# Optimization experiments

Measured on AMD Instinct MI355X. Metric: run time of the kernel, lower is better.

The kernel has to match this reference:

```python
import jax, jax.numpy as jnp
import numpy as np

HIDDEN = 256
NUM_STEPS = 3
N_NODES = 200000
N_GRAPHS = 512


def setup_inputs() -> dict:
    key = jax.random.key(0)
    ks = jax.random.split(key, 8)
    h = HIDDEN
    x = jax.random.normal(ks[0], (N_NODES, h), dtype=jnp.float32)
    batch = jnp.sort(jax.random.randint(ks[1], (N_NODES,), 0, N_GRAPHS)).astype(jnp.int64)
    s_ih = 1.0 / np.sqrt(2 * h)
    s_hh = 1.0 / np.sqrt(h)
    # LSTM (input 2h -> hidden h), PyTorch gate order i,f,g,o
    W_ih = jax.random.uniform(ks[2], (4 * h, 2 * h), jnp.float32, -s_ih, s_ih)
    W_hh = jax.random.uniform(ks[3], (4 * h, h), jnp.float32, -s_hh, s_hh)
    b_ih = jax.random.uniform(ks[4], (4 * h,), jnp.float32, -s_hh, s_hh)
    b_hh = jax.random.uniform(ks[5], (4 * h,), jnp.float32, -s_hh, s_hh)
    # out_proj: Linear(2h -> h)
    s_o = 1.0 / np.sqrt(2 * h)
    W_out = jax.random.uniform(ks[6], (h, 2 * h), jnp.float32, -s_o, s_o)
    b_out = jax.random.uniform(ks[7], (h,), jnp.float32, -s_o, s_o)
    return {"x": x, "batch": batch, "W_ih": W_ih, "W_hh": W_hh,
            "b_ih": b_ih, "b_hh": b_hh, "W_out": W_out, "b_out": b_out,
            "n_graphs": N_GRAPHS}


def _set2set(x, batch, W_ih, W_hh, b_ih, b_hh, n_graphs):
    h = x.shape[1]
    hs = jnp.zeros((n_graphs, h), x.dtype)
    cs = jnp.zeros((n_graphs, h), x.dtype)
    q_star = jnp.zeros((n_graphs, 2 * h), x.dtype)
    for _ in range(NUM_STEPS):
        # LSTM step (PyTorch gate order: i, f, g, o)
        gates = q_star @ W_ih.T + hs @ W_hh.T + (b_ih + b_hh)  # [B, 4h]
        i_g, f_g, g_g, o_g = jnp.split(gates, 4, axis=-1)
        cs = jax.nn.sigmoid(f_g) * cs + jax.nn.sigmoid(i_g) * jnp.tanh(g_g)
        hs = jax.nn.sigmoid(o_g) * jnp.tanh(cs)
        q = hs  # [B, h]
        # attention logits per node
        e = jnp.sum(x * q[batch], axis=-1)  # [N]
        # segment softmax over nodes of each graph
        m = jax.ops.segment_max(e, batch, num_segments=n_graphs)
        a = jnp.exp(e - m[batch])
        denom = jax.ops.segment_sum(a, batch, num_segments=n_graphs)
        a = a / denom[batch]
        # weighted readout
        r = jax.ops.segment_sum(a[:, None] * x, batch, num_segments=n_graphs)  # [B, h]
        q_star = jnp.concatenate([q, r], axis=-1)  # [B, 2h]
    return q_star


def reference(x, batch, W_ih, W_hh, b_ih, b_hh, W_out, b_out, n_graphs):
    q_star = _set2set(x, batch.astype(jnp.int32), W_ih, W_hh, b_ih, b_hh, n_graphs)
    return q_star @ W_out.T + b_out
```

## Files before the change

kernel.cpp:

```cpp
#include <hip/hip_runtime.h>
#include <hip/hip_bf16.h>

#define HID 256
#define NG 512

__device__ __forceinline__ float sigmoidf_(float v) { return 1.f / (1.f + __expf(-v)); }

__global__ __launch_bounds__(256) void prep_kernel(
    const float* __restrict__ W_ih, const float* __restrict__ W_hh,
    const float* __restrict__ b_ih, const float* __restrict__ b_hh,
    float* __restrict__ Wcat, float* __restrict__ bcat)
{
    int idx = blockIdx.x * 256 + threadIdx.x;
    if (idx < 1024 * 512) {
        int k = idx & 511;
        float v = W_ih[idx];
        if (k < 256) v += W_hh[(idx >> 9) * 256 + k];
        Wcat[idx] = v;
    }
    if (idx < 1024) bcat[idx] = b_ih[idx] + b_hh[idx];
}

__global__ __launch_bounds__(256) void find_starts(
    const int* __restrict__ batch, int n, int* __restrict__ starts)
{
    int g = blockIdx.x * 256 + threadIdx.x;
    if (g > NG) return;
    if (g == NG) { starts[NG] = n; return; }
    int lo = 0, hi = n;
    while (lo < hi) {
        int mid = (lo + hi) >> 1;
        if (batch[mid] < g) lo = mid + 1; else hi = mid;
    }
    starts[g] = lo;
}

__global__ __launch_bounds__(256) void attn_kernel(
    const float* __restrict__ x, const int* __restrict__ starts,
    const float* __restrict__ gp0, const float* __restrict__ gp1,
    const float* __restrict__ bcat, float* __restrict__ cs,
    float* __restrict__ qs, int step0)
{
    __shared__ __align__(16) float ql[HID];
    __shared__ __align__(16) float red[4][HID];
    __shared__ float mw[4], lw[4];

    const int g = blockIdx.x;
    const int tid = threadIdx.x;

    float ig, fg, gg, og, cp;
    if (step0) {
        ig = bcat[tid]; fg = bcat[256 + tid]; gg = bcat[512 + tid]; og = bcat[768 + tid];
        cp = 0.f;
    } else {
        const float* a0 = gp0 + (size_t)g * 1024;
        const float* a1 = gp1 + (size_t)g * 1024;
        ig = a0[tid]       + a1[tid]       + bcat[tid];
        fg = a0[256 + tid] + a1[256 + tid] + bcat[256 + tid];
        gg = a0[512 + tid] + a1[512 + tid] + bcat[512 + tid];
        og = a0[768 + tid] + a1[768 + tid] + bcat[768 + tid];
        cp = cs[g * HID + tid];
    }
    float cn = sigmoidf_(fg) * cp + sigmoidf_(ig) * tanhf(gg);
    float h  = sigmoidf_(og) * tanhf(cn);
    cs[g * HID + tid] = cn;
    qs[(size_t)g * 512 + tid] = h;
    ql[tid] = h;

    const int s0 = starts[g];
    const int nn = starts[g + 1] - s0;
    if (nn <= 0) { qs[(size_t)g * 512 + HID + tid] = 0.f; return; }
    __syncthreads();

    const int w = tid >> 6, lane = tid & 63;
    const int j = lane >> 3;
    const int s = lane & 7;

    float4 qf[8];
    #pragma unroll
    for (int k = 0; k < 8; ++k) qf[k] = *(const float4*)&ql[k * 32 + s * 4];

    const int nch = (nn + 7) >> 3;
    const int last = s0 + nn - 1;
    const float NEG = -3.402823466e38f;

    float m_run = NEG, l_run = 0.f;
    float4 racc[8] = {};
    float4 xc[8], xn[8];

    int c = w;
    if (c < nch) {
        int node = s0 + c * 8 + j; if (node > last) node = last;
        const float* bp = x + (size_t)node * HID + s * 4;
        #pragma unroll
        for (int k = 0; k < 8; ++k) xc[k] = *(const float4*)(bp + k * 32);
    }
    for (; c < nch; c += 4) {
        if (c + 4 < nch) {
            int node = s0 + (c + 4) * 8 + j; if (node > last) node = last;
            const float* bp = x + (size_t)node * HID + s * 4;
            #pragma unroll
            for (int k = 0; k < 8; ++k) xn[k] = *(const float4*)(bp + k * 32);
        }
        const bool valid = (c * 8 + j) < nn;

        float e = 0.f;
        #pragma unroll
        for (int k = 0; k < 8; ++k)
            e += xc[k].x * qf[k].x + xc[k].y * qf[k].y + xc[k].z * qf[k].z + xc[k].w * qf[k].w;
        e += __shfl_xor(e, 1); e += __shfl_xor(e, 2); e += __shfl_xor(e, 4);
        e = valid ? e : NEG;

        float mc = e;
        mc = fmaxf(mc, __shfl_xor(mc, 8));
        mc = fmaxf(mc, __shfl_xor(mc, 16));
        mc = fmaxf(mc, __shfl_xor(mc, 32));
        float m_new = fmaxf(m_run, mc);
        float alpha = __expf(m_run - m_new);
        float p = valid ? __expf(e - m_new) : 0.f;
        float ps = p;
        ps += __shfl_xor(ps, 8); ps += __shfl_xor(ps, 16); ps += __shfl_xor(ps, 32);
        l_run = l_run * alpha + ps;
        m_run = m_new;
        #pragma unroll
        for (int k = 0; k < 8; ++k) {
            racc[k].x = racc[k].x * alpha + p * xc[k].x;
            racc[k].y = racc[k].y * alpha + p * xc[k].y;
            racc[k].z = racc[k].z * alpha + p * xc[k].z;
            racc[k].w = racc[k].w * alpha + p * xc[k].w;
        }
        #pragma unroll
        for (int k = 0; k < 8; ++k) xc[k] = xn[k];
    }

    #pragma unroll
    for (int k = 0; k < 8; ++k) {
        racc[k].x += __shfl_xor(racc[k].x, 8);
        racc[k].y += __shfl_xor(racc[k].y, 8);
        racc[k].z += __shfl_xor(racc[k].z, 8);
        racc[k].w += __shfl_xor(racc[k].w, 8);
        racc[k].x += __shfl_xor(racc[k].x, 16);
        racc[k].y += __shfl_xor(racc[k].y, 16);
        racc[k].z += __shfl_xor(racc[k].z, 16);
        racc[k].w += __shfl_xor(racc[k].w, 16);
        racc[k].x += __shfl_xor(racc[k].x, 32);
        racc[k].y += __shfl_xor(racc[k].y, 32);
        racc[k].z += __shfl_xor(racc[k].z, 32);
        racc[k].w += __shfl_xor(racc[k].w, 32);
    }
    if (j == 0) {
        #pragma unroll
        for (int k = 0; k < 8; ++k) *(float4*)&red[w][k * 32 + s * 4] = racc[k];
        if (s == 0) { mw[w] = m_run; lw[w] = l_run; }
    }
    __syncthreads();

    float M = fmaxf(fmaxf(mw[0], mw[1]), fmaxf(mw[2], mw[3]));
    float f0 = __expf(mw[0] - M), f1 = __expf(mw[1] - M);
    float f2 = __expf(mw[2] - M), f3 = __expf(mw[3] - M);
    float L = lw[0] * f0 + lw[1] * f1 + lw[2] * f2 + lw[3] * f3;
    float r = red[0][tid] * f0 + red[1][tid] * f1 + red[2][tid] * f2 + red[3][tid] * f3;
    qs[(size_t)g * 512 + HID + tid] = r / L;
}

__global__ __launch_bounds__(256) void gemm_splitk(
    const float* __restrict__ A, int lda,
    const float* __restrict__ B, int ldb,
    float* __restrict__ Cp, int ldc, int KS, size_t slice_stride)
{
    __shared__ float As[16][76];
    __shared__ float Bs[16][76];
    const int tid = threadIdx.x;
    const int tx = tid & 15, ty = tid >> 4;
    const int m0 = blockIdx.y * 64, n0 = blockIdx.x * 64;
    const int kb = blockIdx.z * KS;
    const int r = tid >> 2, kc = (tid & 3) << 2;
    float acc[4][4] = {};

    const float* Ap = &A[(size_t)(m0 + r) * lda + kb + kc];
    const float* Bp = &B[(size_t)(n0 + r) * ldb + kb + kc];
    float4 av = *(const float4*)Ap;
    float4 bv = *(const float4*)Bp;

    for (int k0 = 0; k0 < KS; k0 += 16) {
        As[kc + 0][r] = av.x; As[kc + 1][r] = av.y; As[kc + 2][r] = av.z; As[kc + 3][r] = av.w;
        Bs[kc + 0][r] = bv.x; Bs[kc + 1][r] = bv.y; Bs[kc + 2][r] = bv.z; Bs[kc + 3][r] = bv.w;
        __syncthreads();
        if (k0 + 16 < KS) {
            av = *(const float4*)(Ap + k0 + 16);
            bv = *(const float4*)(Bp + k0 + 16);
        }
        #pragma unroll
        for (int kk = 0; kk < 16; ++kk) {
            float4 a = *(const float4*)&As[kk][ty << 2];
            float4 b = *(const float4*)&Bs[kk][tx << 2];
            acc[0][0] += a.x * b.x; acc[0][1] += a.x * b.y; acc[0][2] += a.x * b.z; acc[0][3] += a.x * b.w;
            acc[1][0] += a.y * b.x; acc[1][1] += a.y * b.y; acc[1][2] += a.y * b.z; acc[1][3] += a.y * b.w;
            acc[2][0] += a.z * b.x; acc[2][1] += a.z * b.y; acc[2][2] += a.z * b.z; acc[2][3] += a.z * b.w;
            acc[3][0] += a.w * b.x; acc[3][1] += a.w * b.y; acc[3][2] += a.w * b.z; acc[3][3] += a.w * b.w;
        }
        __syncthreads();
    }
    float* out = Cp + blockIdx.z * slice_stride;
    #pragma unroll
    for (int i = 0; i < 4; ++i) {
        float4 o = make_float4(acc[i][0], acc[i][1], acc[i][2], acc[i][3]);
        *(float4*)&out[(size_t)(m0 + ty * 4 + i) * ldc + n0 + (tx << 2)] = o;
    }
}

__global__ __launch_bounds__(256) void finalize_out(
    const float* __restrict__ op, const float* __restrict__ b_out,
    float* __restrict__ out)
{
    int i = blockIdx.x * 256 + threadIdx.x;
    if (i < 512 * 256) {
        float v = op[i] + op[131072 + i] + op[262144 + i] + op[393216 + i] + b_out[i & 255];
        out[i] = v;
    }
}

extern "C" void kernel_launch(void* const* d_in, const int* in_sizes, int n_in,
                              void* d_out, int out_size, void* d_ws, size_t ws_size,
                              hipStream_t stream)
{
    const float* x     = (const float*)d_in[0];
    const int*   batch = (const int*)d_in[1];
    const float* W_ih  = (const float*)d_in[2];
    const float* W_hh  = (const float*)d_in[3];
    const float* b_ih  = (const float*)d_in[4];
    const float* b_hh  = (const float*)d_in[5];
    const float* W_out = (const float*)d_in[6];
    const float* b_out = (const float*)d_in[7];
    float* out = (float*)d_out;
    const int n = in_sizes[1];
    (void)n_in; (void)out_size; (void)ws_size;

    char* ws = (char*)d_ws;
    float* qs      = (float*)(ws);
    float* cs      = (float*)(ws + 0x100000);
    float* gates_p = (float*)(ws + 0x180000);
    float* Wcat    = (float*)(ws + 0x580000);
    float* bcat    = (float*)(ws + 0x780000);
    int*   starts  = (int*)  (ws + 0x781000);
    float* out_p   = (float*)(ws + 0x790000);

    prep_kernel<<<2048, 256, 0, stream>>>(W_ih, W_hh, b_ih, b_hh, Wcat, bcat);
    find_starts<<<3, 256, 0, stream>>>(batch, n, starts);

    for (int step = 0; step < 3; ++step) {
        if (step > 0) {
            gemm_splitk<<<dim3(16, 8, 2), 256, 0, stream>>>(
                qs, 512, Wcat, 512, gates_p, 1024, 256, (size_t)512 * 1024);
        }
        attn_kernel<<<NG, 256, 0, stream>>>(
            x, starts, gates_p, gates_p + (size_t)512 * 1024, bcat, cs, qs, step == 0);
    }
    gemm_splitk<<<dim3(4, 8, 4), 256, 0, stream>>>(
        qs, 512, W_out, 512, out_p, 256, 128, (size_t)512 * 256);
    finalize_out<<<512, 256, 0, stream>>>(out_p, b_out, out);
}
```

Measured before the change: 415.3 us.

## Double attention block to 512 threads, split gate GEMM 4-way, merge setup kernels

The attention kernel now runs 8 wavefronts per graph instead of 4. Each wave streams every eighth chunk of nodes, and an 8-way online-softmax merge combines the partial results. To free registers, the query vector is read from shared memory inside the dot product instead of being kept in registers. The gate GEMM split-K goes from 2 to 4 slices to expose more blocks, the workspace is reshuffled to fit four partial slices, and the two setup kernels are merged into one launch. The extra waves should hide more memory latency per graph, at the cost of more LDS reads, a larger reduction and more partial-sum traffic.

```diff
diff --git a/kernel.cpp b/kernel.cpp
--- a/kernel.cpp
+++ b/kernel.cpp
@@ -1,84 +1,86 @@
 #include <hip/hip_runtime.h>
-#include <hip/hip_bf16.h>
 
 #define HID 256
 #define NG 512
 
 __device__ __forceinline__ float sigmoidf_(float v) { return 1.f / (1.f + __expf(-v)); }
 
-__global__ __launch_bounds__(256) void prep_kernel(
+__global__ __launch_bounds__(256) void setup_kernel(
     const float* __restrict__ W_ih, const float* __restrict__ W_hh,
     const float* __restrict__ b_ih, const float* __restrict__ b_hh,
-    float* __restrict__ Wcat, float* __restrict__ bcat)
-{
-    int idx = blockIdx.x * 256 + threadIdx.x;
-    if (idx < 1024 * 512) {
+    float* __restrict__ Wcat, float* __restrict__ bcat,
+    const int* __restrict__ batch, int n, int* __restrict__ starts)
+{
+    int b = blockIdx.x;
+    if (b < 2048) {
+        int idx = b * 256 + threadIdx.x;
         int k = idx & 511;
         float v = W_ih[idx];
         if (k < 256) v += W_hh[(idx >> 9) * 256 + k];
         Wcat[idx] = v;
-    }
-    if (idx < 1024) bcat[idx] = b_ih[idx] + b_hh[idx];
-}
-
-__global__ __launch_bounds__(256) void find_starts(
-    const int* __restrict__ batch, int n, int* __restrict__ starts)
-{
-    int g = blockIdx.x * 256 + threadIdx.x;
-    if (g > NG) return;
-    if (g == NG) { starts[NG] = n; return; }
-    int lo = 0, hi = n;
-    while (lo < hi) {
-        int mid = (lo + hi) >> 1;
-        if (batch[mid] < g) lo = mid + 1; else hi = mid;
-    }
-    starts[g] = lo;
-}
-
-__global__ __launch_bounds__(256) void attn_kernel(
+        if (idx < 1024) bcat[idx] = b_ih[idx] + b_hh[idx];
+    } else {
+        int g = (b - 2048) * 256 + threadIdx.x;
+        if (g > NG) return;
+        if (g == NG) { starts[NG] = n; return; }
+        int lo = 0, hi = n;
+        while (lo < hi) {
+            int mid = (lo + hi) >> 1;
+            if (batch[mid] < g) lo = mid + 1; else hi = mid;
+        }
+        starts[g] = lo;
+    }
+}
+
+__global__ __launch_bounds__(512, 4) void attn_kernel(
     const float* __restrict__ x, const int* __restrict__ starts,
-    const float* __restrict__ gp0, const float* __restrict__ gp1,
+    const float* __restrict__ gates_p,
     const float* __restrict__ bcat, float* __restrict__ cs,
     float* __restrict__ qs, int step0)
 {
     __shared__ __align__(16) float ql[HID];
-    __shared__ __align__(16) float red[4][HID];
-    __shared__ float mw[4], lw[4];
+    __shared__ __align__(16) float red[8][HID];
+    __shared__ float mw[8], lw[8];
 
     const int g = blockIdx.x;
     const int tid = threadIdx.x;
 
-    float ig, fg, gg, og, cp;
-    if (step0) {
-        ig = bcat[tid]; fg = bcat[256 + tid]; gg = bcat[512 + tid]; og = bcat[768 + tid];
-        cp = 0.f;
-    } else {
-        const float* a0 = gp0 + (size_t)g * 1024;
-        const float* a1 = gp1 + (size_t)g * 1024;
-        ig = a0[tid]       + a1[tid]       + bcat[tid];
-        fg = a0[256 + tid] + a1[256 + tid] + bcat[256 + tid];
-        gg = a0[512 + tid] + a1[512 + tid] + bcat[512 + tid];
-        og = a0[768 + tid] + a1[768 + tid] + bcat[768 + tid];
-        cp = cs[g * HID + tid];
-    }
-    float cn = sigmoidf_(fg) * cp + sigmoidf_(ig) * tanhf(gg);
-    float h  = sigmoidf_(og) * tanhf(cn);
-    cs[g * HID + tid] = cn;
-    qs[(size_t)g * 512 + tid] = h;
-    ql[tid] = h;
+    if (tid < 256) {
+        float ig, fg, gg, og, cp;
+        if (step0) {
+            ig = bcat[tid]; fg = bcat[256 + tid]; gg = bcat[512 + tid]; og = bcat[768 + tid];
+            cp = 0.f;
+        } else {
+            ig = bcat[tid]; fg = bcat[256 + tid]; gg = bcat[512 + tid]; og = bcat[768 + tid];
+            const float* a = gates_p + (size_t)g * 1024;
+            const size_t ss = (size_t)512 * 1024;
+            #pragma unroll
+            for (int z = 0; z < 4; ++z) {
+                const float* az = a + z * ss;
+                ig += az[tid]; fg += az[256 + tid]; gg += az[512 + tid]; og += az[768 + tid];
+            }
+            cp = cs[g * HID + tid];
+        }
+        float cn = sigmoidf_(fg) * cp + sigmoidf_(ig) * tanhf(gg);
+        float h  = sigmoidf_(og) * tanhf(cn);
+        cs[g * HID + tid] = cn;
+        qs[(size_t)g * 512 + tid] = h;
+        ql[tid] = h;
+    }
+    __syncthreads();
 
     const int s0 = starts[g];
     const int nn = starts[g + 1] - s0;
-    if (nn <= 0) { qs[(size_t)g * 512 + HID + tid] = 0.f; return; }
-    __syncthreads();
+    if (nn <= 0) {
+        if (tid < 256) qs[(size_t)g * 512 + HID + tid] = 0.f;
+        return;
+    }
 
     const int w = tid >> 6, lane = tid & 63;
     const int j = lane >> 3;
     const int s = lane & 7;
 
-    float4 qf[8];
-    #pragma unroll
-    for (int k = 0; k < 8; ++k) qf[k] = *(const float4*)&ql[k * 32 + s * 4];
+    const float4* qp = (const float4*)&ql[s * 4];
 
     const int nch = (nn + 7) >> 3;
     const int last = s0 + nn - 1;
@@ -95,9 +97,9 @@
         #pragma unroll
         for (int k = 0; k < 8; ++k) xc[k] = *(const float4*)(bp + k * 32);
     }
-    for (; c < nch; c += 4) {
-        if (c + 4 < nch) {
-            int node = s0 + (c + 4) * 8 + j; if (node > last) node = last;
+    for (; c < nch; c += 8) {
+        if (c + 8 < nch) {
+            int node = s0 + (c + 8) * 8 + j; if (node > last) node = last;
             const float* bp = x + (size_t)node * HID + s * 4;
             #pragma unroll
             for (int k = 0; k < 8; ++k) xn[k] = *(const float4*)(bp + k * 32);
@@ -106,8 +108,10 @@
 
         float e = 0.f;
         #pragma unroll
-        for (int k = 0; k < 8; ++k)
-            e += xc[k].x * qf[k].x + xc[k].y * qf[k].y + xc[k].z * qf[k].z + xc[k].w * qf[k].w;
+        for (int k = 0; k < 8; ++k) {
+            float4 q = qp[k * 8];
+            e += xc[k].x * q.x + xc[k].y * q.y + xc[k].z * q.z + xc[k].w * q.w;
+        }
         e += __shfl_xor(e, 1); e += __shfl_xor(e, 2); e += __shfl_xor(e, 4);
         e = valid ? e : NEG;
 
@@ -155,12 +159,19 @@
     }
     __syncthreads();
 
-    float M = fmaxf(fmaxf(mw[0], mw[1]), fmaxf(mw[2], mw[3]));
-    float f0 = __expf(mw[0] - M), f1 = __expf(mw[1] - M);
-    float f2 = __expf(mw[2] - M), f3 = __expf(mw[3] - M);
-    float L = lw[0] * f0 + lw[1] * f1 + lw[2] * f2 + lw[3] * f3;
-    float r = red[0][tid] * f0 + red[1][tid] * f1 + red[2][tid] * f2 + red[3][tid] * f3;
-    qs[(size_t)g * 512 + HID + tid] = r / L;
+    if (tid < 256) {
+        float M = NEG;
+        #pragma unroll
+        for (int v = 0; v < 8; ++v) M = fmaxf(M, mw[v]);
+        float L = 0.f, r = 0.f;
+        #pragma unroll
+        for (int v = 0; v < 8; ++v) {
+            float f = __expf(mw[v] - M);
+            L += lw[v] * f;
+            r += red[v][tid] * f;
+        }
+        qs[(size_t)g * 512 + HID + tid] = r / L;
+    }
 }
 
 __global__ __launch_bounds__(256) void gemm_splitk(
@@ -240,21 +251,21 @@
     float* qs      = (float*)(ws);
     float* cs      = (float*)(ws + 0x100000);
     float* gates_p = (float*)(ws + 0x180000);
-    float* Wcat    = (float*)(ws + 0x580000);
-    float* bcat    = (float*)(ws + 0x780000);
-    int*   starts  = (int*)  (ws + 0x781000);
-    float* out_p   = (float*)(ws + 0x790000);
-
-    prep_kernel<<<2048, 256, 0, stream>>>(W_ih, W_hh, b_ih, b_hh, Wcat, bcat);
-    find_starts<<<3, 256, 0, stream>>>(batch, n, starts);
+    float* Wcat    = (float*)(ws + 0x980000);
+    float* bcat    = (float*)(ws + 0xB80000);
+    int*   starts  = (int*)  (ws + 0xB81000);
+    float* out_p   = (float*)(ws + 0xB90000);
+
+    setup_kernel<<<2051, 256, 0, stream>>>(W_ih, W_hh, b_ih, b_hh, Wcat, bcat,
+                                           batch, n, starts);
 
     for (int step = 0; step < 3; ++step) {
         if (step > 0) {
-            gemm_splitk<<<dim3(16, 8, 2), 256, 0, stream>>>(
-                qs, 512, Wcat, 512, gates_p, 1024, 256, (size_t)512 * 1024);
-        }
-        attn_kernel<<<NG, 256, 0, stream>>>(
-            x, starts, gates_p, gates_p + (size_t)512 * 1024, bcat, cs, qs, step == 0);
+            gemm_splitk<<<dim3(16, 8, 4), 256, 0, stream>>>(
+                qs, 512, Wcat, 512, gates_p, 1024, 128, (size_t)512 * 1024);
+        }
+        attn_kernel<<<NG, 512, 0, stream>>>(
+            x, starts, gates_p, bcat, cs, qs, step == 0);
     }
     gemm_splitk<<<dim3(4, 8, 4), 256, 0, stream>>>(
         qs, 512, W_out, 512, out_p, 256, 128, (size_t)512 * 256);
```

Result: slower. 491.2 us (+18.3%).

## Split fused online-softmax attention into separate logit, softmax and readout kernels

Applied to the files above, without the earlier changes.

Replaces the single-pass online-softmax attention kernel with three kernels. The first computes per-node logits, the second does the segment max and sum and writes normalized weights, and the third accumulates the weighted readout. This removes the per-chunk rescaling and shuffle reductions from the inner loop. In exchange x is read twice per step, two extra launches are added per step, and e/a buffers make a round trip through memory. Prep and find_starts are also merged into one setup kernel to drop a launch.

```diff
diff --git a/kernel.cpp b/kernel.cpp
--- a/kernel.cpp
+++ b/kernel.cpp
@@ -1,75 +1,70 @@
 #include <hip/hip_runtime.h>
-#include <hip/hip_bf16.h>
 
 #define HID 256
 #define NG 512
 
 __device__ __forceinline__ float sigmoidf_(float v) { return 1.f / (1.f + __expf(-v)); }
 
-__global__ __launch_bounds__(256) void prep_kernel(
+__global__ __launch_bounds__(256) void setup_kernel(
     const float* __restrict__ W_ih, const float* __restrict__ W_hh,
     const float* __restrict__ b_ih, const float* __restrict__ b_hh,
-    float* __restrict__ Wcat, float* __restrict__ bcat)
-{
-    int idx = blockIdx.x * 256 + threadIdx.x;
-    if (idx < 1024 * 512) {
+    float* __restrict__ Wcat, float* __restrict__ bcat,
+    const int* __restrict__ batch, int n, int* __restrict__ starts)
+{
+    int b = blockIdx.x;
+    if (b < 2048) {
+        int idx = b * 256 + threadIdx.x;
         int k = idx & 511;
         float v = W_ih[idx];
         if (k < 256) v += W_hh[(idx >> 9) * 256 + k];
         Wcat[idx] = v;
-    }
-    if (idx < 1024) bcat[idx] = b_ih[idx] + b_hh[idx];
-}
-
-__global__ __launch_bounds__(256) void find_starts(
-    const int* __restrict__ batch, int n, int* __restrict__ starts)
-{
-    int g = blockIdx.x * 256 + threadIdx.x;
-    if (g > NG) return;
-    if (g == NG) { starts[NG] = n; return; }
-    int lo = 0, hi = n;
-    while (lo < hi) {
-        int mid = (lo + hi) >> 1;
-        if (batch[mid] < g) lo = mid + 1; else hi = mid;
-    }
-    starts[g] = lo;
-}
-
-__global__ __launch_bounds__(256) void attn_kernel(
+        if (idx < 1024) bcat[idx] = b_ih[idx] + b_hh[idx];
+    } else {
+        int g = (b - 2048) * 256 + threadIdx.x;
+        if (g > NG) return;
+        if (g == NG) { starts[NG] = n; return; }
+        int lo = 0, hi = n;
+        while (lo < hi) {
+            int mid = (lo + hi) >> 1;
+            if (batch[mid] < g) lo = mid + 1; else hi = mid;
+        }
+        starts[g] = lo;
+    }
+}
+
+__global__ __launch_bounds__(256) void e_kernel(
     const float* __restrict__ x, const int* __restrict__ starts,
-    const float* __restrict__ gp0, const float* __restrict__ gp1,
+    const float* __restrict__ gates_p,
     const float* __restrict__ bcat, float* __restrict__ cs,
-    float* __restrict__ qs, int step0)
+    float* __restrict__ qs, float* __restrict__ e, int step0)
 {
     __shared__ __align__(16) float ql[HID];
-    __shared__ __align__(16) float red[4][HID];
-    __shared__ float mw[4], lw[4];
 
     const int g = blockIdx.x;
     const int tid = threadIdx.x;
 
-    float ig, fg, gg, og, cp;
-    if (step0) {
-        ig = bcat[tid]; fg = bcat[256 + tid]; gg = bcat[512 + tid]; og = bcat[768 + tid];
-        cp = 0.f;
-    } else {
-        const float* a0 = gp0 + (size_t)g * 1024;
-        const float* a1 = gp1 + (size_t)g * 1024;
-        ig = a0[tid]       + a1[tid]       + bcat[tid];
-        fg = a0[256 + tid] + a1[256 + tid] + bcat[256 + tid];
-        gg = a0[512 + tid] + a1[512 + tid] + bcat[512 + tid];
-        og = a0[768 + tid] + a1[768 + tid] + bcat[768 + tid];
-        cp = cs[g * HID + tid];
-    }
-    float cn = sigmoidf_(fg) * cp + sigmoidf_(ig) * tanhf(gg);
-    float h  = sigmoidf_(og) * tanhf(cn);
-    cs[g * HID + tid] = cn;
-    qs[(size_t)g * 512 + tid] = h;
-    ql[tid] = h;
+    {
+        float ig = bcat[tid], fg = bcat[256 + tid], gg = bcat[512 + tid], og = bcat[768 + tid];
+        float cp = 0.f;
+        if (!step0) {
+            const float* a0 = gates_p + (size_t)g * 1024;
+            const float* a1 = a0 + (size_t)512 * 1024;
+            ig += a0[tid]       + a1[tid];
+            fg += a0[256 + tid] + a1[256 + tid];
+            gg += a0[512 + tid] + a1[512 + tid];
+            og += a0[768 + tid] + a1[768 + tid];
+            cp = cs[g * HID + tid];
+        }
+        float cn = sigmoidf_(fg) * cp + sigmoidf_(ig) * tanhf(gg);
+        float h  = sigmoidf_(og) * tanhf(cn);
+        cs[g * HID + tid] = cn;
+        qs[(size_t)g * 512 + tid] = h;
+        ql[tid] = h;
+    }
 
     const int s0 = starts[g];
     const int nn = starts[g + 1] - s0;
-    if (nn <= 0) { qs[(size_t)g * 512 + HID + tid] = 0.f; return; }
+    if (nn <= 0) return;
     __syncthreads();
 
     const int w = tid >> 6, lane = tid & 63;
@@ -82,12 +77,8 @@
 
     const int nch = (nn + 7) >> 3;
     const int last = s0 + nn - 1;
-    const float NEG = -3.402823466e38f;
-
-    float m_run = NEG, l_run = 0.f;
-    float4 racc[8] = {};
+
     float4 xc[8], xn[8];
-
     int c = w;
     if (c < nch) {
         int node = s0 + c * 8 + j; if (node > last) node = last;
@@ -102,35 +93,96 @@
             #pragma unroll
             for (int k = 0; k < 8; ++k) xn[k] = *(const float4*)(bp + k * 32);
         }
-        const bool valid = (c * 8 + j) < nn;
-
-        float e = 0.f;
+        float ev = 0.f;
         #pragma unroll
         for (int k = 0; k < 8; ++k)
-            e += xc[k].x * qf[k].x + xc[k].y * qf[k].y + xc[k].z * qf[k].z + xc[k].w * qf[k].w;
-        e += __shfl_xor(e, 1); e += __shfl_xor(e, 2); e += __shfl_xor(e, 4);
-        e = valid ? e : NEG;
-
-        float mc = e;
-        mc = fmaxf(mc, __shfl_xor(mc, 8));
-        mc = fmaxf(mc, __shfl_xor(mc, 16));
-        mc = fmaxf(mc, __shfl_xor(mc, 32));
-        float m_new = fmaxf(m_run, mc);
-        float alpha = __expf(m_run - m_new);
-        float p = valid ? __expf(e - m_new) : 0.f;
-        float ps = p;
-        ps += __shfl_xor(ps, 8); ps += __shfl_xor(ps, 16); ps += __shfl_xor(ps, 32);
-        l_run = l_run * alpha + ps;
-        m_run = m_new;
+            ev += xc[k].x * qf[k].x + xc[k].y * qf[k].y + xc[k].z * qf[k].z + xc[k].w * qf[k].w;
+        ev += __shfl_xor(ev, 1); ev += __shfl_xor(ev, 2); ev += __shfl_xor(ev, 4);
+        if (s == 0 && (c * 8 + j) < nn) e[s0 + c * 8 + j] = ev;
+        #pragma unroll
+        for (int k = 0; k < 8; ++k) xc[k] = xn[k];
+    }
+}
+
+__global__ __launch_bounds__(256) void s_kernel(
+    const float* __restrict__ e, const int* __restrict__ starts,
+    float* __restrict__ a)
+{
+    __shared__ float sm[4], sl[4];
+    const int g = blockIdx.x, tid = threadIdx.x;
+    const int s0 = starts[g];
+    const int nn = starts[g + 1] - s0;
+    if (nn <= 0) return;
+    const int w = tid >> 6, lane = tid & 63;
+
+    float m = -3.402823466e38f;
+    for (int i = tid; i < nn; i += 256) m = fmaxf(m, e[s0 + i]);
+    m = fmaxf(m, __shfl_xor(m, 1));  m = fmaxf(m, __shfl_xor(m, 2));
+    m = fmaxf(m, __shfl_xor(m, 4));  m = fmaxf(m, __shfl_xor(m, 8));
+    m = fmaxf(m, __shfl_xor(m, 16)); m = fmaxf(m, __shfl_xor(m, 32));
+    if (lane == 0) sm[w] = m;
+    __syncthreads();
+    const float M = fmaxf(fmaxf(sm[0], sm[1]), fmaxf(sm[2], sm[3]));
+
+    float l = 0.f;
+    for (int i = tid; i < nn; i += 256) l += __expf(e[s0 + i] - M);
+    l += __shfl_xor(l, 1);  l += __shfl_xor(l, 2);  l += __shfl_xor(l, 4);
+    l += __shfl_xor(l, 8);  l += __shfl_xor(l, 16); l += __shfl_xor(l, 32);
+    if (lane == 0) sl[w] = l;
+    __syncthreads();
+    const float L = sl[0] + sl[1] + sl[2] + sl[3];
+
+    const float inv = 1.f / L;
+    for (int i = tid; i < nn; i += 256) a[s0 + i] = __expf(e[s0 + i] - M) * inv;
+}
+
+__global__ __launch_bounds__(256) void r_kernel(
+    const float* __restrict__ x, const int* __restrict__ starts,
+    const float* __restrict__ a, float* __restrict__ qs)
+{
+    __shared__ __align__(16) float red[4][HID];
+    const int g = blockIdx.x, tid = threadIdx.x;
+    const int s0 = starts[g];
+    const int nn = starts[g + 1] - s0;
+    if (nn <= 0) { qs[(size_t)g * 512 + HID + tid] = 0.f; return; }
+
+    const int w = tid >> 6, lane = tid & 63;
+    const int j = lane >> 3;
+    const int s = lane & 7;
+    const int nch = (nn + 7) >> 3;
+    const int last = s0 + nn - 1;
+
+    float4 racc[8] = {};
+    float4 xc[8], xn[8];
+    float ac = 0.f, an = 0.f;
+
+    int c = w;
+    if (c < nch) {
+        int node = s0 + c * 8 + j; if (node > last) node = last;
+        const float* bp = x + (size_t)node * HID + s * 4;
+        #pragma unroll
+        for (int k = 0; k < 8; ++k) xc[k] = *(const float4*)(bp + k * 32);
+        ac = a[node];
+    }
+    for (; c < nch; c += 4) {
+        if (c + 4 < nch) {
+            int node = s0 + (c + 4) * 8 + j; if (node > last) node = last;
+            const float* bp = x + (size_t)node * HID + s * 4;
+            #pragma unroll
+            for (int k = 0; k < 8; ++k) xn[k] = *(const float4*)(bp + k * 32);
+            an = a[node];
+        }
+        const float p = ((c * 8 + j) < nn) ? ac : 0.f;
         #pragma unroll
         for (int k = 0; k < 8; ++k) {
-            racc[k].x = racc[k].x * alpha + p * xc[k].x;
-            racc[k].y = racc[k].y * alpha + p * xc[k].y;
-            racc[k].z = racc[k].z * alpha + p * xc[k].z;
-            racc[k].w = racc[k].w * alpha + p * xc[k].w;
+            racc[k].x += p * xc[k].x;
+            racc[k].y += p * xc[k].y;
+            racc[k].z += p * xc[k].z;
+            racc[k].w += p * xc[k].w;
         }
         #pragma unroll
         for (int k = 0; k < 8; ++k) xc[k] = xn[k];
+        ac = an;
     }
 
     #pragma unroll
@@ -151,16 +203,10 @@
     if (j == 0) {
         #pragma unroll
         for (int k = 0; k < 8; ++k) *(float4*)&red[w][k * 32 + s * 4] = racc[k];
-        if (s == 0) { mw[w] = m_run; lw[w] = l_run; }
     }
     __syncthreads();
-
-    float M = fmaxf(fmaxf(mw[0], mw[1]), fmaxf(mw[2], mw[3]));
-    float f0 = __expf(mw[0] - M), f1 = __expf(mw[1] - M);
-    float f2 = __expf(mw[2] - M), f3 = __expf(mw[3] - M);
-    float L = lw[0] * f0 + lw[1] * f1 + lw[2] * f2 + lw[3] * f3;
-    float r = red[0][tid] * f0 + red[1][tid] * f1 + red[2][tid] * f2 + red[3][tid] * f3;
-    qs[(size_t)g * 512 + HID + tid] = r / L;
+    qs[(size_t)g * 512 + HID + tid] =
+        red[0][tid] + red[1][tid] + red[2][tid] + red[3][tid];
 }
 
 __global__ __launch_bounds__(256) void gemm_splitk(
@@ -243,18 +289,22 @@
     float* Wcat    = (float*)(ws + 0x580000);
     float* bcat    = (float*)(ws + 0x780000);
     int*   starts  = (int*)  (ws + 0x781000);
-    float* out_p   = (float*)(ws + 0x790000);
-
-    prep_kernel<<<2048, 256, 0, stream>>>(W_ih, W_hh, b_ih, b_hh, Wcat, bcat);
-    find_starts<<<3, 256, 0, stream>>>(batch, n, starts);
+    float* e_buf   = (float*)(ws + 0x790000);
+    float* a_buf   = (float*)(ws + 0x860000);
+    float* out_p   = (float*)(ws + 0x930000);
+
+    setup_kernel<<<2051, 256, 0, stream>>>(W_ih, W_hh, b_ih, b_hh, Wcat, bcat,
+                                           batch, n, starts);
 
     for (int step = 0; step < 3; ++step) {
         if (step > 0) {
             gemm_splitk<<<dim3(16, 8, 2), 256, 0, stream>>>(
                 qs, 512, Wcat, 512, gates_p, 1024, 256, (size_t)512 * 1024);
         }
-        attn_kernel<<<NG, 256, 0, stream>>>(
-            x, starts, gates_p, gates_p + (size_t)512 * 1024, bcat, cs, qs, step == 0);
+        e_kernel<<<NG, 256, 0, stream>>>(x, starts, gates_p, bcat, cs, qs,
+                                         e_buf, step == 0);
+        s_kernel<<<NG, 256, 0, stream>>>(e_buf, starts, a_buf);
+        r_kernel<<<NG, 256, 0, stream>>>(x, starts, a_buf, qs);
     }
     gemm_splitk<<<dim3(4, 8, 4), 256, 0, stream>>>(
         qs, 512, W_out, 512, out_p, 256, 128, (size_t)512 * 256);
```

After: 514.8 us. 1.24x slower.
